# Kernel tuning notes

Hardware: AMD Instinct MI355X
Metric: run time of the kernel (lower is better)

The kernel has to match this reference:

```python
import jax, jax.numpy as jnp
import numpy as np

B, T, C, H, D, K = 2, 2048, 1024, 16, 64, 4
INNER = H * D
EPS = 1e-6


def l2_norm(x):
    return x * jax.lax.rsqrt(jnp.sum(x * x, axis=-1, keepdims=True) + EPS)


def rms_norm(x):
    return x * jax.lax.rsqrt(jnp.mean(x * x, axis=-1, keepdims=True) + EPS)


def conv_silu(x, w, b):
    # causal depthwise conv1d + SiLU; x: [B,T,inner], w: [inner,1,K], b: [inner]
    xc = jnp.transpose(x, (0, 2, 1))
    xc = jnp.pad(xc, ((0, 0), (0, 0), (K - 1, 0)))
    xc = jax.lax.conv_general_dilated(
        xc, w.astype(xc.dtype), window_strides=(1,), padding='VALID',
        dimension_numbers=('NCW', 'OIW', 'NCW'), feature_group_count=xc.shape[1])
    xc = xc + b.astype(xc.dtype)[:, None]
    return jnp.transpose(jax.nn.silu(xc), (0, 2, 1))


def setup_inputs() -> dict:
    key = jax.random.key(0)
    ks = jax.random.split(key, 16)

    def lin(k, o, i):
        return jax.random.normal(k, (o, i), jnp.float32) / np.float32(np.sqrt(i))

    dt_min, dt_max = 0.001, 0.1
    dt = jnp.exp(jax.random.uniform(ks[12], (H,)) * (np.log(dt_max) - np.log(dt_min)) + np.log(dt_min))
    return {
        'x': jax.random.normal(ks[0], (B, T, C), jnp.float32),
        'wq': lin(ks[1], INNER, C), 'wk': lin(ks[2], INNER, C),
        'wv': lin(ks[3], INNER, C), 'wg': lin(ks[4], INNER, C),
        'wo': lin(ks[5], C, INNER),
        'wa': lin(ks[6], H, C), 'wb': lin(ks[7], H, C),
        'conv_q_w': jax.random.normal(ks[8], (INNER, 1, K)) * 0.02, 'conv_q_b': jnp.zeros(INNER),
        'conv_k_w': jax.random.normal(ks[9], (INNER, 1, K)) * 0.02, 'conv_k_b': jnp.zeros(INNER),
        'conv_v_w': jax.random.normal(ks[10], (INNER, 1, K)) * 0.02, 'conv_v_b': jnp.zeros(INNER),
        'A_log': jnp.log(jax.random.uniform(ks[11], (H,), minval=0.0, maxval=16.0) + 1e-6),
        'dt_bias': dt + jnp.log(-jnp.expm1(-dt)),
        'o_norm_scale': jnp.ones(D),
    }


def reference(x, wq, wk, wv, wg, wo, wa, wb,
              conv_q_w, conv_q_b, conv_k_w, conv_k_b, conv_v_w, conv_v_b,
              A_log, dt_bias, o_norm_scale):
    q = conv_silu(x @ wq.T, conv_q_w, conv_q_b).reshape(B, T, H, D)
    k = conv_silu(x @ wk.T, conv_k_w, conv_k_b).reshape(B, T, H, D)
    v = conv_silu(x @ wv.T, conv_v_w, conv_v_b).reshape(B, T, H, D)
    g_out = (x @ wg.T).reshape(B, T, H, D)

    q = l2_norm(q)
    k = l2_norm(k)

    beta = jax.nn.sigmoid(x @ wb.T)                     # [B,T,H]
    a = x @ wa.T + dt_bias                              # [B,T,H]
    decay = jnp.exp(-jnp.exp(A_log) * jax.nn.softplus(a))

    # time-major for scan
    q_T = jnp.transpose(q, (1, 0, 2, 3))
    k_T = jnp.transpose(k, (1, 0, 2, 3))
    v_T = jnp.transpose(v, (1, 0, 2, 3))
    beta_T = jnp.transpose(beta, (1, 0, 2))
    decay_T = jnp.transpose(decay, (1, 0, 2))

    def step(S_prev, xs):
        q_t, k_t, v_t, beta_t, decay_t = xs
        kS = jnp.einsum('bhd,bhde->bhe', k_t, S_prev)
        delta = v_t - kS
        write = beta_t[..., None, None] * jnp.einsum('bhd,bhe->bhde', k_t, delta)
        S_new = decay_t[..., None, None] * S_prev + write
        o_t = jnp.einsum('bhd,bhde->bhe', q_t, S_new)
        return S_new, o_t

    S_init = jnp.zeros((B, H, D, D), dtype=x.dtype)
    _, o_T = jax.lax.scan(step, S_init, (q_T, k_T, v_T, beta_T, decay_T))

    o = jnp.transpose(o_T, (1, 0, 2, 3))                # [B,T,H,D]
    o = rms_norm(o) * o_norm_scale
    o = o * jax.nn.silu(g_out)
    return o.reshape(B, T, INNER) @ wo.T
```

## Files before the change

### kernel.cpp

```cpp
#include <hip/hip_runtime.h>
#include <math.h>

#define BB 2
#define TT 2048
#define CC 1024
#define HH 16
#define DD 64
#define INNER 1024
#define BT (BB*TT)
#define EPSF 1e-6f
#define CH 64
#define NC (TT/CH)
#define NBH (BB*HH)
#define NCHK (NBH*NC)

typedef unsigned short u16;
typedef __bf16 bf16x8 __attribute__((ext_vector_type(8)));
typedef float f32x4 __attribute__((ext_vector_type(4)));

__device__ inline u16 f2bf(float f) {
  unsigned u = __builtin_bit_cast(unsigned, f);
  return (u16)((u + 0x7fffu + ((u >> 16) & 1u)) >> 16);
}
__device__ inline float b2f(u16 b) {
  unsigned u = ((unsigned)b) << 16;
  return __builtin_bit_cast(float, u);
}
__device__ inline void gll16(const u16* g, u16* l) {
  __builtin_amdgcn_global_load_lds(
      (const __attribute__((address_space(1))) void*)g,
      (__attribute__((address_space(3))) void*)l, 16, 0, 0);
}

__device__ u16   g_pqb[BT * INNER];
__device__ u16   g_pkb[BT * INNER];
__device__ u16   g_pvb[BT * INNER];
__device__ u16   g_qb [BT * INNER];
__device__ u16   g_kb [BT * INNER];
__device__ u16   g_vb [BT * INNER];
__device__ u16   g_gb [BT * INNER];
__device__ u16   g_ob [BT * INNER];
__device__ float g_beta[BT * HH];
__device__ float g_ldec[BT * HH];
__device__ u16   g_xb[BT * CC];
__device__ u16   g_wbb[4 * INNER * CC];
__device__ u16   g_wob[CC * INNER];
__device__ u16   g_gatedb[BT * INNER];
__device__ u16   g_U0 [NCHK * CH * DD];
__device__ u16   g_Wt [NCHK * DD * CH];
__device__ u16   g_Bt [NCHK * CH * CH];
__device__ u16   g_Qht[NCHK * DD * CH];
__device__ float g_Mc [NCHK * DD * DD];
__device__ float g_bc [NCHK * DD * DD];
__device__ float g_Sall[NCHK * DD * DD];

__global__ __launch_bounds__(256) void cast_all(
    const float* __restrict__ x, const float* __restrict__ wq,
    const float* __restrict__ wk, const float* __restrict__ wv,
    const float* __restrict__ wg, const float* __restrict__ wo,
    u16* __restrict__ xb, u16* __restrict__ wb, u16* __restrict__ wob) {
  long i = ((long)blockIdx.x * 256 + threadIdx.x) * 4;
  const float* src;
  u16* dst;
  if (i < 4194304)      { src = x  + i;             dst = xb + i; }
  else if (i < 5242880) { src = wq + (i - 4194304); dst = wb + (i - 4194304); }
  else if (i < 6291456) { src = wk + (i - 5242880); dst = wb + (i - 4194304); }
  else if (i < 7340032) { src = wv + (i - 6291456); dst = wb + (i - 4194304); }
  else if (i < 8388608) { src = wg + (i - 7340032); dst = wb + (i - 4194304); }
  else                  { src = wo + (i - 8388608); dst = wob + (i - 8388608); }
  float4 v = *(const float4*)src;
  ushort4 o;
  o.x = f2bf(v.x); o.y = f2bf(v.y); o.z = f2bf(v.z); o.w = f2bf(v.w);
  *(ushort4*)dst = o;
}

template <typename OutT, int NBN>
__global__ __launch_bounds__(256) void bgemm4(
    const u16* __restrict__ A, const u16* __restrict__ B,
    OutT* __restrict__ c0, OutT* __restrict__ c1,
    OutT* __restrict__ c2, OutT* __restrict__ c3) {
  __shared__ u16 lA[128 * 64];
  __shared__ u16 lB[128 * 64];
  const int tid = threadIdx.x;
  const int bid = blockIdx.x;
  int bm, bn;
  if constexpr (NBN == 32) {
    const int xcd = bid & 7;
    const int idx = bid >> 3;
    const int in_ = idx >> 4;
    int im = idx & 15;
    im = (in_ & 1) ? (15 - im) : im;
    bm = ((xcd >> 2) * 16 + im) * 128;
    bn = ((xcd & 3) * 8 + in_) * 128;
  } else {
    const int xcd = bid & 7;
    const int idx = bid >> 3;
    const int in_ = idx >> 2;
    int im = idx & 3;
    im = (in_ & 1) ? (3 - im) : im;
    bm = (xcd * 4 + im) * 128;
    bn = in_ * 128;
  }
  const int lane = tid & 63;
  const int wave = tid >> 6;
  const int wr = (wave >> 1) * 64, wc = (wave & 1) * 64;
  const int lr = lane & 15;
  const int kq = lane >> 4;
  const int srow0 = tid >> 3;
  const int gcol = ((tid & 7) ^ (srow0 & 7)) * 8;
  const u16* gA0 = &A[(long)(bm + srow0) * CC + gcol];
  const u16* gB0 = &B[(long)(bn + srow0) * CC + gcol];
  u16* lA0 = &lA[tid * 8];
  u16* lB0 = &lB[tid * 8];
  f32x4 acc[4][4] = {};

  for (int k0 = 0; k0 < CC; k0 += 64) {
    __syncthreads();
#pragma unroll
    for (int p = 0; p < 4; ++p) {
      gll16(gA0 + (long)p * 32 * CC + k0, lA0 + p * 2048);
      gll16(gB0 + (long)p * 32 * CC + k0, lB0 + p * 2048);
    }
    __syncthreads();
#pragma unroll
    for (int ks = 0; ks < 2; ++ks) {
      const int sl = ((ks * 4 + kq) ^ (lr & 7)) * 8;
      bf16x8 af[4], bf_[4];
#pragma unroll
      for (int m = 0; m < 4; ++m)
        af[m] = __builtin_bit_cast(bf16x8,
            *(const uint4*)&lA[(wr + m * 16 + lr) * 64 + sl]);
#pragma unroll
      for (int n = 0; n < 4; ++n)
        bf_[n] = __builtin_bit_cast(bf16x8,
            *(const uint4*)&lB[(wc + n * 16 + lr) * 64 + sl]);
#pragma unroll
      for (int m = 0; m < 4; ++m)
#pragma unroll
        for (int n = 0; n < 4; ++n)
          acc[m][n] = __builtin_amdgcn_mfma_f32_16x16x32_bf16(
              af[m], bf_[n], acc[m][n], 0, 0, 0);
    }
  }
  OutT* cp = (bn < 1024) ? c0 : (bn < 2048) ? c1 : (bn < 3072) ? c2 : c3;
  const int ccol0 = (bn & 1023) + wc;
  const int crow0 = bm + wr + kq * 4;
#pragma unroll
  for (int m = 0; m < 4; ++m)
#pragma unroll
    for (int n = 0; n < 4; ++n) {
      int col = ccol0 + n * 16 + lr;
#pragma unroll
      for (int r = 0; r < 4; ++r) {
        long idx2 = (long)(crow0 + m * 16 + r) * INNER + col;
        if constexpr (sizeof(OutT) == 2) cp[idx2] = f2bf(acc[m][n][r]);
        else                             cp[idx2] = acc[m][n][r];
      }
    }
}

__global__ __launch_bounds__(256) void conv3(
    const u16* __restrict__ pq, const u16* __restrict__ pk,
    const u16* __restrict__ pv,
    const float* __restrict__ cqw, const float* __restrict__ cqb,
    const float* __restrict__ ckw, const float* __restrict__ ckb,
    const float* __restrict__ cvw, const float* __restrict__ cvb,
    u16* __restrict__ oq, u16* __restrict__ ok, u16* __restrict__ ov) {
  const int which = blockIdx.y;
  const u16* pre = which == 0 ? pq : which == 1 ? pk : pv;
  const float* cw = which == 0 ? cqw : which == 1 ? ckw : cvw;
  const float* cb = which == 0 ? cqb : which == 1 ? ckb : cvb;
  u16* out = which == 0 ? oq : which == 1 ? ok : ov;
  const int do_l2 = (which < 2);

  const int bt = blockIdx.x;
  const int b = bt / TT, t = bt % TT;
  const int tid = threadIdx.x;
  const int c4 = tid * 4;
  float xt[4][4];
#pragma unroll
  for (int j = 0; j < 4; ++j) {
    int ts = t - 3 + j;
    if (ts >= 0) {
      ushort4 u = *(const ushort4*)&pre[(long)(b * TT + ts) * INNER + c4];
      xt[j][0] = b2f(u.x); xt[j][1] = b2f(u.y);
      xt[j][2] = b2f(u.z); xt[j][3] = b2f(u.w);
    } else {
      xt[j][0] = xt[j][1] = xt[j][2] = xt[j][3] = 0.f;
    }
  }
  float4 bias4 = *(const float4*)&cb[c4];
  const float* bp = (const float*)&bias4;
  float y[4];
#pragma unroll
  for (int ci = 0; ci < 4; ++ci) {
    float4 w4 = *(const float4*)&cw[(c4 + ci) * 4];
    float acc = bp[ci];
    acc += w4.x * xt[0][ci];
    acc += w4.y * xt[1][ci];
    acc += w4.z * xt[2][ci];
    acc += w4.w * xt[3][ci];
    y[ci] = acc / (1.f + expf(-acc));
  }
  if (do_l2) {
    float ssq = y[0]*y[0] + y[1]*y[1] + y[2]*y[2] + y[3]*y[3];
    ssq += __shfl_xor(ssq, 1);
    ssq += __shfl_xor(ssq, 2);
    ssq += __shfl_xor(ssq, 4);
    ssq += __shfl_xor(ssq, 8);
    float r = rsqrtf(ssq + EPSF);
    y[0] *= r; y[1] *= r; y[2] *= r; y[3] *= r;
  }
  ushort4 res;
  res.x = f2bf(y[0]); res.y = f2bf(y[1]);
  res.z = f2bf(y[2]); res.w = f2bf(y[3]);
  *(ushort4*)&out[(long)bt * INNER + c4] = res;
}

__global__ __launch_bounds__(256) void proj_ab3(
    const float* __restrict__ x, const float* __restrict__ wa,
    const float* __restrict__ wb, const float* __restrict__ dt_bias,
    const float* __restrict__ A_log, float* __restrict__ beta,
    float* __restrict__ ldec) {
  const int m0 = blockIdx.x * 8;
  const int tid = threadIdx.x;
  __shared__ float xs[8][132];
  __shared__ float ws[32][132];
  const int row = tid >> 5;
  const int col = tid & 31;
  float a0 = 0.f, a1 = 0.f, a2 = 0.f, a3 = 0.f;
  const int sxr = tid >> 5, sxc = (tid & 31) * 4;
  for (int k0 = 0; k0 < CC; k0 += 128) {
    __syncthreads();
    *(float4*)&xs[sxr][sxc] = *(const float4*)&x[(long)(m0 + sxr) * CC + k0 + sxc];
#pragma unroll
    for (int p = 0; p < 4; ++p) {
      int idx = tid + p * 256;
      int wr = idx >> 5, wc4 = (idx & 31) * 4;
      const float* wsrc = (wr < 16) ? &wa[(long)wr * CC] : &wb[(long)(wr - 16) * CC];
      *(float4*)&ws[wr][wc4] = *(const float4*)&wsrc[k0 + wc4];
    }
    __syncthreads();
#pragma unroll
    for (int kk = 0; kk < 128; kk += 16) {
      float4 x0 = *(const float4*)&xs[row][kk + 0];
      float4 w0 = *(const float4*)&ws[col][kk + 0];
      float4 x1 = *(const float4*)&xs[row][kk + 4];
      float4 w1 = *(const float4*)&ws[col][kk + 4];
      float4 x2 = *(const float4*)&xs[row][kk + 8];
      float4 w2 = *(const float4*)&ws[col][kk + 8];
      float4 x3 = *(const float4*)&xs[row][kk + 12];
      float4 w3 = *(const float4*)&ws[col][kk + 12];
      a0 += x0.x * w0.x + x0.y * w0.y + x0.z * w0.z + x0.w * w0.w;
      a1 += x1.x * w1.x + x1.y * w1.y + x1.z * w1.z + x1.w * w1.w;
      a2 += x2.x * w2.x + x2.y * w2.y + x2.z * w2.z + x2.w * w2.w;
      a3 += x3.x * w3.x + x3.y * w3.y + x3.z * w3.z + x3.w * w3.w;
    }
  }
  float acc = (a0 + a1) + (a2 + a3);
  const int m = m0 + row;
  if (col < 16) {
    float a = acc + dt_bias[col];
    float sp = fmaxf(a, 0.f) + log1pf(expf(-fabsf(a)));
    ldec[(long)m * HH + col] = -expf(A_log[col]) * sp;
  } else {
    beta[(long)m * HH + (col - 16)] = 1.f / (1.f + expf(-acc));
  }
}

__global__ __launch_bounds__(256) void gdn_prep(
    const u16* __restrict__ q, const u16* __restrict__ k,
    const u16* __restrict__ v, const float* __restrict__ beta,
    const float* __restrict__ ldec,
    u16* __restrict__ U0g, u16* __restrict__ Wtg, u16* __restrict__ Btg,
    u16* __restrict__ Qhtg, float* __restrict__ Mtg, float* __restrict__ bvg) {
  const int blk = blockIdx.x;
  const int bh = blk / NC, c = blk % NC;
  const int b = bh >> 4, h = bh & 15;
  const int tid = threadIdx.x;
  const int tx = tid & 15, ty = tid >> 4;
  __shared__ float P0[64][68];
  __shared__ float P1[64][68];
  __shared__ float Ab[64][68];
  __shared__ float lam[64], lamx[64], lbet[64];
  const long gb = ((long)(b * TT + c * CH) * HH + h) * DD;

  {
    const int e4 = (tid & 15) * 4;
    const int t0 = tid >> 4;
#pragma unroll
    for (int p = 0; p < 4; ++p) {
      int t = t0 + p * 16;
      ushort4 qv = *(const ushort4*)&q[gb + (long)t * (HH * DD) + e4];
      P1[e4 + 0][t] = b2f(qv.x); P1[e4 + 1][t] = b2f(qv.y);
      P1[e4 + 2][t] = b2f(qv.z); P1[e4 + 3][t] = b2f(qv.w);
    }
  }
  float ldv = 0.f, bv_ = 0.f;
  if (tid < 64) {
    ldv = ldec[(long)(b * TT + c * CH + tid) * HH + h];
    bv_ = beta[(long)(b * TT + c * CH + tid) * HH + h];
    lam[tid] = ldv;
  }
  __syncthreads();
  float lsum = 0.f;
  if (tid < 64) {
    for (int s = 0; s <= tid; ++s) lsum += lam[s];
  }
  __syncthreads();
  if (tid < 64) {
    lam[tid] = lsum;
    lamx[tid] = lsum - ldv;
    lbet[tid] = bv_;
  }
  __syncthreads();

  {
    const int lane = tid & 63;
    const int wave = tid >> 6;
    const int lr = lane & 15;
    const int kq = lane >> 4;
    const int mwr = (wave >> 1) * 32, mwc = (wave & 1) * 32;
    bf16x8 af[2][2], bk_[2][2], bq_[2][2];
#pragma unroll
    for (int m = 0; m < 2; ++m)
#pragma unroll
      for (int ks = 0; ks < 2; ++ks) {
        long rbase = gb + (long)(mwr + m * 16 + lr) * (HH * DD) + ks * 32 + kq * 8;
        long cbase = gb + (long)(mwc + m * 16 + lr) * (HH * DD) + ks * 32 + kq * 8;
        af[m][ks]  = __builtin_bit_cast(bf16x8, *(const uint4*)&k[rbase]);
        bk_[m][ks] = __builtin_bit_cast(bf16x8, *(const uint4*)&k[cbase]);
        bq_[m][ks] = __builtin_bit_cast(bf16x8, *(const uint4*)&q[cbase]);
      }
    f32x4 gf[2][2] = {}, pf[2][2] = {};
#pragma unroll
    for (int ks = 0; ks < 2; ++ks)
#pragma unroll
      for (int m = 0; m < 2; ++m)
#pragma unroll
        for (int n = 0; n < 2; ++n) {
          gf[m][n] = __builtin_amdgcn_mfma_f32_16x16x32_bf16(
              af[m][ks], bk_[n][ks], gf[m][n], 0, 0, 0);
          pf[m][n] = __builtin_amdgcn_mfma_f32_16x16x32_bf16(
              af[m][ks], bq_[n][ks], pf[m][n], 0, 0, 0);
        }
    u16* btp = Btg + (long)blk * (CH * CH);
#pragma unroll
    for (int m = 0; m < 2; ++m)
#pragma unroll
      for (int n = 0; n < 2; ++n)
#pragma unroll
        for (int r = 0; r < 4; ++r) {
          int t = mwr + m * 16 + kq * 4 + r;
          int s = mwc + n * 16 + lr;
          Ab[t][s] = (s < t) ? lbet[t] * expf(lamx[t] - lam[s]) * gf[m][n][r]
                             : 0.f;
          btp[t * 64 + s] = f2bf(
              (t <= s) ? expf(lam[s] - lam[t]) * pf[m][n][r] : 0.f);
        }
  }
  {
    u16* qhp = Qhtg + (long)blk * (DD * CH);
    const int t4 = (tid & 15) * 4;
    const int d0 = tid >> 4;
#pragma unroll
    for (int p = 0; p < 4; ++p) {
      int d = d0 + p * 16;
      float4 qv = *(const float4*)&P1[d][t4];
      ushort4 qw;
      qw.x = f2bf(qv.x * expf(lam[t4 + 0]));
      qw.y = f2bf(qv.y * expf(lam[t4 + 1]));
      qw.z = f2bf(qv.z * expf(lam[t4 + 2]));
      qw.w = f2bf(qv.w * expf(lam[t4 + 3]));
      *(ushort4*)&qhp[d * 64 + t4] = qw;
    }
  }
  __syncthreads();
  {
    const int e4 = (tid & 15) * 4;
    const int t0 = tid >> 4;
#pragma unroll
    for (int p = 0; p < 4; ++p) {
      int t = t0 + p * 16;
      float bt_ = lbet[t], cx = bt_ * expf(lamx[t]);
      ushort4 vv4 = *(const ushort4*)&v[gb + (long)t * (HH * DD) + e4];
      ushort4 kv4 = *(const ushort4*)&k[gb + (long)t * (HH * DD) + e4];
      float4 vv = make_float4(b2f(vv4.x) * bt_, b2f(vv4.y) * bt_,
                              b2f(vv4.z) * bt_, b2f(vv4.w) * bt_);
      float4 kv = make_float4(b2f(kv4.x) * cx, b2f(kv4.y) * cx,
                              b2f(kv4.z) * cx, b2f(kv4.w) * cx);
      *(float4*)&P0[t][e4] = vv;
      *(float4*)&P1[t][e4] = kv;
    }
  }
  __syncthreads();
  {
    const int i = tid >> 5;
    const int j4 = (tid & 31) * 4;
    float* Pj = (j4 < 64) ? (&P0[0][0] + j4) : (&P1[0][0] + (j4 - 64));
#pragma unroll
    for (int base = 0; base < 64; base += 8) {
      const int r = base + i;
      float4 acc = *(const float4*)&Pj[r * 68];
      for (int t = 0; t < base; ++t) {
        float a = Ab[r][t];
        float4 ut = *(const float4*)&Pj[t * 68];
        acc.x -= a * ut.x; acc.y -= a * ut.y;
        acc.z -= a * ut.z; acc.w -= a * ut.w;
      }
      *(float4*)&Pj[r * 68] = acc;
      __syncthreads();
      float4 val[8];
#pragma unroll
      for (int t = 0; t < 8; ++t) {
        float4 vt = *(const float4*)&Pj[(base + t) * 68];
#pragma unroll
        for (int m = 0; m < t; ++m) {
          float a = Ab[base + t][base + m];
          vt.x -= a * val[m].x; vt.y -= a * val[m].y;
          vt.z -= a * val[m].z; vt.w -= a * val[m].w;
        }
        val[t] = vt;
      }
      float4 fin = val[0];
#pragma unroll
      for (int t = 1; t < 8; ++t) if (i == t) fin = val[t];
      __syncthreads();
      *(float4*)&Pj[r * 68] = fin;
      __syncthreads();
    }
  }
  {
    u16* u0p = U0g + (long)blk * (CH * DD);
    const int e4 = (tid & 15) * 4;
    const int t0 = tid >> 4;
    float lamL = lam[63];
#pragma unroll
    for (int p = 0; p < 4; ++p) {
      int t = t0 + p * 16;
      float4 u4 = *(const float4*)&P0[t][e4];
      ushort4 uw;
      uw.x = f2bf(u4.x); uw.y = f2bf(u4.y);
      uw.z = f2bf(u4.z); uw.w = f2bf(u4.w);
      *(ushort4*)&u0p[t * 64 + e4] = uw;
      float cf = expf(lamL - lam[t]);
      ushort4 kv4 = *(const ushort4*)&k[gb + (long)t * (HH * DD) + e4];
      *(float4*)&Ab[t][e4] = make_float4(b2f(kv4.x) * cf, b2f(kv4.y) * cf,
                                         b2f(kv4.z) * cf, b2f(kv4.w) * cf);
    }
    u16* wtp = Wtg + (long)blk * (DD * CH);
    const int t = tid & 63;
    const int d0 = tid >> 6;
#pragma unroll
    for (int p = 0; p < 16; ++p) {
      int d = d0 + p * 4;
      wtp[d * 64 + t] = f2bf(P1[t][d]);
    }
  }
  __syncthreads();
  {
    float accm[4][4] = {}, accb[4][4] = {};
    for (int t = 0; t < 64; ++t) {
      float4 ka = *(const float4*)&Ab[t][ty * 4];
      float4 wc_ = *(const float4*)&P1[t][tx * 4];
      float4 uv = *(const float4*)&P0[t][tx * 4];
      float kar[4] = {ka.x, ka.y, ka.z, ka.w};
      float wcr[4] = {wc_.x, wc_.y, wc_.z, wc_.w};
      float ucr[4] = {uv.x, uv.y, uv.z, uv.w};
#pragma unroll
      for (int i = 0; i < 4; ++i)
#pragma unroll
        for (int j = 0; j < 4; ++j) {
          accm[i][j] += kar[i] * wcr[j];
          accb[i][j] += kar[i] * ucr[j];
        }
    }
    float gLv = expf(lam[63]);
    float* mp = Mtg + (long)blk * (DD * DD);
    float* bp = bvg + (long)blk * (DD * DD);
#pragma unroll
    for (int i = 0; i < 4; ++i) {
      int rr = ty * 4 + i;
      float4 mv, b4;
      mv.x = ((rr == tx * 4 + 0) ? gLv : 0.f) - accm[i][0];
      mv.y = ((rr == tx * 4 + 1) ? gLv : 0.f) - accm[i][1];
      mv.z = ((rr == tx * 4 + 2) ? gLv : 0.f) - accm[i][2];
      mv.w = ((rr == tx * 4 + 3) ? gLv : 0.f) - accm[i][3];
      *(float4*)&mp[rr * 64 + tx * 4] = mv;
      b4.x = accb[i][0]; b4.y = accb[i][1];
      b4.z = accb[i][2]; b4.w = accb[i][3];
      *(float4*)&bp[rr * 64 + tx * 4] = b4;
    }
  }
}

__global__ __launch_bounds__(256) void gdn_seq4(
    const float* __restrict__ Mtg, const float* __restrict__ bvg,
    float* __restrict__ Sall) {
  const int bh = blockIdx.x & 31;
  const int esec = blockIdx.x >> 5;
  const int tid = threadIdx.x;
  const int d = tid & 63;
  const int ep = (tid >> 6) * 2;
  const int eo = esec * 8 + ep;
  __shared__ float Ms[64][68];
  __shared__ float Ss[8][68];
  float S0 = 0.f, S1 = 0.f;
  const int sr = tid >> 2, sq = (tid & 3) * 16;
  float4 mreg[4];
  {
    const float* mt0 = Mtg + (long)bh * NC * 4096;
#pragma unroll
    for (int p = 0; p < 4; ++p)
      mreg[p] = *(const float4*)&mt0[sr * 64 + sq + p * 4];
  }
  for (int c = 0; c < NC; ++c) {
    const long cb = (long)bh * NC + c;
    float2 bv = *(const float2*)&bvg[cb * 4096 + d * 64 + eo];
    __syncthreads();
#pragma unroll
    for (int p = 0; p < 4; ++p)
      *(float4*)&Ms[sr][sq + p * 4] = mreg[p];
    *(float2*)&Sall[cb * 4096 + d * 64 + eo] = make_float2(S0, S1);
    Ss[ep][d] = S0; Ss[ep + 1][d] = S1;
    __syncthreads();
    if (c + 1 < NC) {
      const float* mtn = Mtg + (cb + 1) * 4096;
#pragma unroll
      for (int p = 0; p < 4; ++p)
        mreg[p] = *(const float4*)&mtn[sr * 64 + sq + p * 4];
    }
    float a0 = bv.x, a1 = bv.y, b0 = 0.f, b1 = 0.f;
#pragma unroll
    for (int sg = 0; sg < 8; ++sg) {
      float4 m4 = *(const float4*)&Ms[d][sg * 4];
      float4 s0 = *(const float4*)&Ss[ep][sg * 4];
      float4 s1 = *(const float4*)&Ss[ep + 1][sg * 4];
      a0 += m4.x * s0.x + m4.y * s0.y + m4.z * s0.z + m4.w * s0.w;
      a1 += m4.x * s1.x + m4.y * s1.y + m4.z * s1.z + m4.w * s1.w;
    }
#pragma unroll
    for (int sg = 8; sg < 16; ++sg) {
      float4 m4 = *(const float4*)&Ms[d][sg * 4];
      float4 s0 = *(const float4*)&Ss[ep][sg * 4];
      float4 s1 = *(const float4*)&Ss[ep + 1][sg * 4];
      b0 += m4.x * s0.x + m4.y * s0.y + m4.z * s0.z + m4.w * s0.w;
      b1 += m4.x * s1.x + m4.y * s1.y + m4.z * s1.z + m4.w * s1.w;
    }
    S0 = a0 + b0; S1 = a1 + b1;
  }
}

__global__ __launch_bounds__(256) void gdn_out(
    const u16* __restrict__ U0g, const u16* __restrict__ Wtg,
    const u16* __restrict__ Btg, const u16* __restrict__ Qhtg,
    const float* __restrict__ Sall, u16* __restrict__ o) {
  const int blk = blockIdx.x;
  const int bh = blk / NC, c = blk % NC;
  const int b = bh >> 4, h = bh & 15;
  const int tid = threadIdx.x;
  const int tx = tid & 15, ty = tid >> 4;
  __shared__ float S[64][64];
  __shared__ float ub[64][64];
  __shared__ float op[64][64];
  const int e4 = (tid & 15) * 4;
  const int t0s = tid >> 4;
  {
    const int r = tid >> 2, qq = (tid & 3) * 16;
#pragma unroll
    for (int p = 0; p < 4; ++p)
      *(float4*)&S[r][qq + p * 4] =
          *(const float4*)&Sall[(long)blk * 4096 + r * 64 + qq + p * 4];
  }
#pragma unroll
  for (int p = 0; p < 4; ++p) {
    int t = t0s + p * 16;
    ushort4 w4 = *(const ushort4*)&Wtg[(long)blk * 4096 + t * 64 + e4];
    *(float4*)&op[t][e4] = make_float4(b2f(w4.x), b2f(w4.y), b2f(w4.z), b2f(w4.w));
  }
  __syncthreads();
  float acc[4][4];
#pragma unroll
  for (int i = 0; i < 4; ++i) {
    ushort4 u4 = *(const ushort4*)&U0g[(long)blk * 4096 + (ty * 4 + i) * 64 + tx * 4];
    acc[i][0] = b2f(u4.x); acc[i][1] = b2f(u4.y);
    acc[i][2] = b2f(u4.z); acc[i][3] = b2f(u4.w);
  }
  for (int d = 0; d < 64; ++d) {
    float4 a4 = *(const float4*)&op[d][ty * 4];
    float4 b4 = *(const float4*)&S[d][tx * 4];
    float ar[4] = {a4.x, a4.y, a4.z, a4.w};
    float br[4] = {b4.x, b4.y, b4.z, b4.w};
#pragma unroll
    for (int i = 0; i < 4; ++i)
#pragma unroll
      for (int j = 0; j < 4; ++j) acc[i][j] -= ar[i] * br[j];
  }
#pragma unroll
  for (int i = 0; i < 4; ++i)
    *(float4*)&ub[ty * 4 + i][tx * 4] =
        make_float4(acc[i][0], acc[i][1], acc[i][2], acc[i][3]);
  __syncthreads();
#pragma unroll
  for (int p = 0; p < 4; ++p) {
    int t = t0s + p * 16;
    ushort4 w4 = *(const ushort4*)&Btg[(long)blk * 4096 + t * 64 + e4];
    *(float4*)&op[t][e4] = make_float4(b2f(w4.x), b2f(w4.y), b2f(w4.z), b2f(w4.w));
  }
  __syncthreads();
  float acco[4][4] = {};
  for (int s = 0; s < 64; ++s) {
    float4 a4 = *(const float4*)&op[s][ty * 4];
    float4 b4 = *(const float4*)&ub[s][tx * 4];
    float ar[4] = {a4.x, a4.y, a4.z, a4.w};
    float br[4] = {b4.x, b4.y, b4.z, b4.w};
#pragma unroll
    for (int i = 0; i < 4; ++i)
#pragma unroll
      for (int j = 0; j < 4; ++j) acco[i][j] += ar[i] * br[j];
  }
  __syncthreads();
#pragma unroll
  for (int p = 0; p < 4; ++p) {
    int t = t0s + p * 16;
    ushort4 w4 = *(const ushort4*)&Qhtg[(long)blk * 4096 + t * 64 + e4];
    *(float4*)&op[t][e4] = make_float4(b2f(w4.x), b2f(w4.y), b2f(w4.z), b2f(w4.w));
  }
  __syncthreads();
  for (int d = 0; d < 64; ++d) {
    float4 a4 = *(const float4*)&op[d][ty * 4];
    float4 b4 = *(const float4*)&S[d][tx * 4];
    float ar[4] = {a4.x, a4.y, a4.z, a4.w};
    float br[4] = {b4.x, b4.y, b4.z, b4.w};
#pragma unroll
    for (int i = 0; i < 4; ++i)
#pragma unroll
      for (int j = 0; j < 4; ++j) acco[i][j] += ar[i] * br[j];
  }
#pragma unroll
  for (int i = 0; i < 4; ++i) {
    int t = ty * 4 + i;
    ushort4 ow;
    ow.x = f2bf(acco[i][0]); ow.y = f2bf(acco[i][1]);
    ow.z = f2bf(acco[i][2]); ow.w = f2bf(acco[i][3]);
    *(ushort4*)&o[((long)(b * TT + c * CH + t) * HH + h) * DD + tx * 4] = ow;
  }
}

__global__ __launch_bounds__(256) void norm_gate(
    const u16* __restrict__ o, const u16* __restrict__ g,
    const float* __restrict__ scale, u16* __restrict__ outb) {
  const int bt = blockIdx.x;
  const int tid = threadIdx.x;
  const int c4 = tid * 4;
  ushort4 o4u = *(const ushort4*)&o[(long)bt * INNER + c4];
  float4 o4 = make_float4(b2f(o4u.x), b2f(o4u.y), b2f(o4u.z), b2f(o4u.w));
  float ssq = o4.x * o4.x + o4.y * o4.y + o4.z * o4.z + o4.w * o4.w;
  ssq += __shfl_xor(ssq, 1);
  ssq += __shfl_xor(ssq, 2);
  ssq += __shfl_xor(ssq, 4);
  ssq += __shfl_xor(ssq, 8);
  float r = rsqrtf(ssq * (1.f / 64.f) + EPSF);
  float4 sc = *(const float4*)&scale[c4 & 63];
  ushort4 g4u = *(const ushort4*)&g[(long)bt * INNER + c4];
  float4 g4 = make_float4(b2f(g4u.x), b2f(g4u.y), b2f(g4u.z), b2f(g4u.w));
  ushort4 res;
  res.x = f2bf(o4.x * r * sc.x * (g4.x / (1.f + expf(-g4.x))));
  res.y = f2bf(o4.y * r * sc.y * (g4.y / (1.f + expf(-g4.y))));
  res.z = f2bf(o4.z * r * sc.z * (g4.z / (1.f + expf(-g4.z))));
  res.w = f2bf(o4.w * r * sc.w * (g4.w / (1.f + expf(-g4.w))));
  *(ushort4*)&outb[(long)bt * INNER + c4] = res;
}

extern "C" void kernel_launch(void* const* d_in, const int* in_sizes, int n_in,
                              void* d_out, int out_size, void* d_ws,
                              size_t ws_size, hipStream_t stream) {
  const float* x      = (const float*)d_in[0];
  const float* wq     = (const float*)d_in[1];
  const float* wk     = (const float*)d_in[2];
  const float* wv     = (const float*)d_in[3];
  const float* wg     = (const float*)d_in[4];
  const float* wo     = (const float*)d_in[5];
  const float* wa     = (const float*)d_in[6];
  const float* wb     = (const float*)d_in[7];
  const float* cqw    = (const float*)d_in[8];
  const float* cqb    = (const float*)d_in[9];
  const float* ckw    = (const float*)d_in[10];
  const float* ckb    = (const float*)d_in[11];
  const float* cvw    = (const float*)d_in[12];
  const float* cvb    = (const float*)d_in[13];
  const float* A_log  = (const float*)d_in[14];
  const float* dtb    = (const float*)d_in[15];
  const float* oscale = (const float*)d_in[16];
  float* out = (float*)d_out;

  u16 *pqb, *pkb, *pvb, *qb, *kb, *vb, *gb, *ob;
  u16 *xb, *wbb, *wob, *gatedb, *U0, *Wt, *Bt, *Qht;
  float *beta, *ldec, *Mc, *bc, *Sall;
  hipGetSymbolAddress((void**)&pqb,   HIP_SYMBOL(g_pqb));
  hipGetSymbolAddress((void**)&pkb,   HIP_SYMBOL(g_pkb));
  hipGetSymbolAddress((void**)&pvb,   HIP_SYMBOL(g_pvb));
  hipGetSymbolAddress((void**)&qb,    HIP_SYMBOL(g_qb));
  hipGetSymbolAddress((void**)&kb,    HIP_SYMBOL(g_kb));
  hipGetSymbolAddress((void**)&vb,    HIP_SYMBOL(g_vb));
  hipGetSymbolAddress((void**)&gb,    HIP_SYMBOL(g_gb));
  hipGetSymbolAddress((void**)&ob,    HIP_SYMBOL(g_ob));
  hipGetSymbolAddress((void**)&beta,  HIP_SYMBOL(g_beta));
  hipGetSymbolAddress((void**)&ldec,  HIP_SYMBOL(g_ldec));
  hipGetSymbolAddress((void**)&xb,    HIP_SYMBOL(g_xb));
  hipGetSymbolAddress((void**)&wbb,   HIP_SYMBOL(g_wbb));
  hipGetSymbolAddress((void**)&wob,   HIP_SYMBOL(g_wob));
  hipGetSymbolAddress((void**)&gatedb,HIP_SYMBOL(g_gatedb));
  hipGetSymbolAddress((void**)&U0,    HIP_SYMBOL(g_U0));
  hipGetSymbolAddress((void**)&Wt,    HIP_SYMBOL(g_Wt));
  hipGetSymbolAddress((void**)&Bt,    HIP_SYMBOL(g_Bt));
  hipGetSymbolAddress((void**)&Qht,   HIP_SYMBOL(g_Qht));
  hipGetSymbolAddress((void**)&Mc,    HIP_SYMBOL(g_Mc));
  hipGetSymbolAddress((void**)&bc,    HIP_SYMBOL(g_bc));
  hipGetSymbolAddress((void**)&Sall,  HIP_SYMBOL(g_Sall));

  cast_all<<<9216, 256, 0, stream>>>(x, wq, wk, wv, wg, wo, xb, wbb, wob);

  bgemm4<u16, 32><<<1024, 256, 0, stream>>>(xb, wbb, pqb, pkb, pvb, gb);

  conv3<<<dim3(BT, 3), 256, 0, stream>>>(pqb, pkb, pvb,
                                         cqw, cqb, ckw, ckb, cvw, cvb,
                                         qb, kb, vb);
  proj_ab3<<<BT / 8, 256, 0, stream>>>(x, wa, wb, dtb, A_log, beta, ldec);

  gdn_prep<<<NCHK, 256, 0, stream>>>(qb, kb, vb, beta, ldec,
                                     U0, Wt, Bt, Qht, Mc, bc);
  gdn_seq4<<<NBH * 8, 256, 0, stream>>>(Mc, bc, Sall);
  gdn_out<<<NCHK, 256, 0, stream>>>(U0, Wt, Bt, Qht, Sall, ob);

  norm_gate<<<BT, 256, 0, stream>>>(ob, gb, oscale, gatedb);

  bgemm4<float, 8><<<256, 256, 0, stream>>>(gatedb, wob, out, out, out, out);
}
```

Before: 294.8 us.

## Split sequential chunk-state scan across more blocks with register-resident M

```diff
diff --git a/kernel.cpp b/kernel.cpp
--- a/kernel.cpp
+++ b/kernel.cpp
@@ -494,60 +494,65 @@
   }
 }
 
-__global__ __launch_bounds__(256) void gdn_seq4(
+__global__ __launch_bounds__(256) void gdn_seq5(
     const float* __restrict__ Mtg, const float* __restrict__ bvg,
     float* __restrict__ Sall) {
   const int bh = blockIdx.x & 31;
   const int esec = blockIdx.x >> 5;
   const int tid = threadIdx.x;
-  const int d = tid & 63;
-  const int ep = (tid >> 6) * 2;
-  const int eo = esec * 8 + ep;
-  __shared__ float Ms[64][68];
-  __shared__ float Ss[8][68];
-  float S0 = 0.f, S1 = 0.f;
-  const int sr = tid >> 2, sq = (tid & 3) * 16;
-  float4 mreg[4];
+  const int lane = tid & 63;
+  const int w = tid >> 6;
+  const int d = w * 16 + (lane & 15);
+  const int q = lane >> 4;
+  const int eo = esec * 4;
+  __shared__ float Ss[4][68];
+  float S0 = 0.f, S1 = 0.f, S2 = 0.f, S3 = 0.f;
+  float4 mreg[4], mnext[4];
+  float4 breg, bnext;
   {
     const float* mt0 = Mtg + (long)bh * NC * 4096;
 #pragma unroll
     for (int p = 0; p < 4; ++p)
-      mreg[p] = *(const float4*)&mt0[sr * 64 + sq + p * 4];
+      mreg[p] = *(const float4*)&mt0[d * 64 + q * 16 + p * 4];
+    breg = *(const float4*)&bvg[(long)bh * NC * 4096 + d * 64 + eo];
   }
   for (int c = 0; c < NC; ++c) {
     const long cb = (long)bh * NC + c;
-    float2 bv = *(const float2*)&bvg[cb * 4096 + d * 64 + eo];
-    __syncthreads();
-#pragma unroll
-    for (int p = 0; p < 4; ++p)
-      *(float4*)&Ms[sr][sq + p * 4] = mreg[p];
-    *(float2*)&Sall[cb * 4096 + d * 64 + eo] = make_float2(S0, S1);
-    Ss[ep][d] = S0; Ss[ep + 1][d] = S1;
+    if (q == 0) {
+      *(float4*)&Sall[cb * 4096 + d * 64 + eo] = make_float4(S0, S1, S2, S3);
+      Ss[0][d] = S0; Ss[1][d] = S1; Ss[2][d] = S2; Ss[3][d] = S3;
+    }
     __syncthreads();
     if (c + 1 < NC) {
       const float* mtn = Mtg + (cb + 1) * 4096;
 #pragma unroll
       for (int p = 0; p < 4; ++p)
-        mreg[p] = *(const float4*)&mtn[sr * 64 + sq + p * 4];
-    }
-    float a0 = bv.x, a1 = bv.y, b0 = 0.f, b1 = 0.f;
-#pragma unroll
-    for (int sg = 0; sg < 8; ++sg) {
-      float4 m4 = *(const float4*)&Ms[d][sg * 4];
-      float4 s0 = *(const float4*)&Ss[ep][sg * 4];
-      float4 s1 = *(const float4*)&Ss[ep + 1][sg * 4];
-      a0 += m4.x * s0.x + m4.y * s0.y + m4.z * s0.z + m4.w * s0.w;
-      a1 += m4.x * s1.x + m4.y * s1.y + m4.z * s1.z + m4.w * s1.w;
-    }
-#pragma unroll
-    for (int sg = 8; sg < 16; ++sg) {
-      float4 m4 = *(const float4*)&Ms[d][sg * 4];
-      float4 s0 = *(const float4*)&Ss[ep][sg * 4];
-      float4 s1 = *(const float4*)&Ss[ep + 1][sg * 4];
-      b0 += m4.x * s0.x + m4.y * s0.y + m4.z * s0.z + m4.w * s0.w;
-      b1 += m4.x * s1.x + m4.y * s1.y + m4.z * s1.z + m4.w * s1.w;
-    }
-    S0 = a0 + b0; S1 = a1 + b1;
+        mnext[p] = *(const float4*)&mtn[d * 64 + q * 16 + p * 4];
+      bnext = *(const float4*)&bvg[(cb + 1) * 4096 + d * 64 + eo];
+    }
+    float p0 = 0.f, p1 = 0.f, p2 = 0.f, p3 = 0.f;
+#pragma unroll
+    for (int j = 0; j < 4; ++j) {
+      float4 m4 = mreg[j];
+      float4 s0 = *(const float4*)&Ss[0][q * 16 + j * 4];
+      float4 s1 = *(const float4*)&Ss[1][q * 16 + j * 4];
+      float4 s2 = *(const float4*)&Ss[2][q * 16 + j * 4];
+      float4 s3 = *(const float4*)&Ss[3][q * 16 + j * 4];
+      p0 += m4.x * s0.x + m4.y * s0.y + m4.z * s0.z + m4.w * s0.w;
+      p1 += m4.x * s1.x + m4.y * s1.y + m4.z * s1.z + m4.w * s1.w;
+      p2 += m4.x * s2.x + m4.y * s2.y + m4.z * s2.z + m4.w * s2.w;
+      p3 += m4.x * s3.x + m4.y * s3.y + m4.z * s3.z + m4.w * s3.w;
+    }
+    p0 += __shfl_xor(p0, 16); p0 += __shfl_xor(p0, 32);
+    p1 += __shfl_xor(p1, 16); p1 += __shfl_xor(p1, 32);
+    p2 += __shfl_xor(p2, 16); p2 += __shfl_xor(p2, 32);
+    p3 += __shfl_xor(p3, 16); p3 += __shfl_xor(p3, 32);
+    S0 = breg.x + p0; S1 = breg.y + p1;
+    S2 = breg.z + p2; S3 = breg.w + p3;
+    __syncthreads();
+    mreg[0] = mnext[0]; mreg[1] = mnext[1];
+    mreg[2] = mnext[2]; mreg[3] = mnext[3];
+    breg = bnext;
   }
 }
 
@@ -730,7 +735,7 @@
 
   gdn_prep<<<NCHK, 256, 0, stream>>>(qb, kb, vb, beta, ldec,
                                      U0, Wt, Bt, Qht, Mc, bc);
-  gdn_seq4<<<NBH * 8, 256, 0, stream>>>(Mc, bc, Sall);
+  gdn_seq5<<<NBH * 16, 256, 0, stream>>>(Mc, bc, Sall);
   gdn_out<<<NCHK, 256, 0, stream>>>(U0, Wt, Bt, Qht, Sall, ob);
 
   norm_gate<<<BT, 256, 0, stream>>>(ob, gb, oscale, gatedb);
```

Result: faster. 273.7 us (-7.1%).
